# Kernel optimization log

Measured on AMD Instinct MI355X. Metric: run time of the kernel, lower is better.

The kernel has to match this reference:

```python
import jax, jax.numpy as jnp
import numpy as np

N_NODES = 100000

def _gcn_conv(x, W, b, src, dst, deg_inv_sqrt):
    # h = X W  (dense GEMM)
    h = x @ W
    # symmetric normalization: norm_e = d^{-1/2}[src] * d^{-1/2}[dst]
    norm = deg_inv_sqrt[src] * deg_inv_sqrt[dst]
    # gather-scale-scatter aggregation
    msgs = h[src] * norm[:, None]
    out = jax.ops.segment_sum(msgs, dst, num_segments=N_NODES)
    return out + b

def _prep_graph(edge_index):
    # add self loops (PyG GCNConv default)
    loop = jnp.arange(N_NODES, dtype=edge_index.dtype)
    src = jnp.concatenate([edge_index[0], loop])
    dst = jnp.concatenate([edge_index[1], loop])
    deg = jax.ops.segment_sum(jnp.ones_like(dst, dtype=jnp.float32), dst,
                              num_segments=N_NODES)
    deg_inv_sqrt = jnp.where(deg > 0, jax.lax.rsqrt(deg), 0.0)
    return src, dst, deg_inv_sqrt

def setup_inputs() -> dict:
    key = jax.random.key(0)
    ks = jax.random.split(key, 5)
    d_in, d_h, d_out, E = 128, 256, 128, 1600000
    x = jax.random.normal(ks[0], (N_NODES, d_in), dtype=jnp.float32)
    edge_index = jax.random.randint(ks[1], (2, E), 0, N_NODES, dtype=jnp.int64)
    W1 = jax.random.normal(ks[2], (d_in, d_h), dtype=jnp.float32) / np.sqrt(d_in)
    W2 = jax.random.normal(ks[3], (d_h, d_h), dtype=jnp.float32) / np.sqrt(d_h)
    W3 = jax.random.normal(ks[4], (d_h, d_out), dtype=jnp.float32) / np.sqrt(d_h)
    return {"x": x, "edge_index": edge_index,
            "W1": W1, "b1": jnp.zeros((d_h,), jnp.float32),
            "W2": W2, "b2": jnp.zeros((d_h,), jnp.float32),
            "W3": W3, "b3": jnp.zeros((d_out,), jnp.float32)}

def reference(x, edge_index, W1, b1, W2, b2, W3, b3):
    src, dst, dis = _prep_graph(edge_index)
    h = _gcn_conv(x, W1, b1, src, dst, dis)
    h = jax.nn.relu(h)  # dropout is identity in eval mode
    h = _gcn_conv(h, W2, b2, src, dst, dis)
    h = jax.nn.relu(h)
    out = _gcn_conv(h, W3, b3, src, dst, dis)
    return out
```

## Files before the change

kernel.cpp:

```cpp
#include <hip/hip_runtime.h>
#include <hip/hip_bf16.h>

#define N_NODES 100000
#define M_PAD   100096
#define SCAN_B  98

typedef __attribute__((ext_vector_type(8))) short s8v;
typedef __attribute__((ext_vector_type(4))) float f4v;
typedef unsigned short u16;
typedef unsigned int   u32;

__device__ __forceinline__ u16 f2bf(float v) {
    __hip_bfloat16 b = __float2bfloat16(v);
    return __builtin_bit_cast(u16, b);
}
__device__ __forceinline__ float bf2f(u16 u) {
    u32 t = (u32)u << 16;
    return __builtin_bit_cast(float, t);
}
__device__ __forceinline__ float bflo(u32 p) { return __builtin_bit_cast(float, p << 16); }
__device__ __forceinline__ float bfhi(u32 p) { return __builtin_bit_cast(float, p & 0xffff0000u); }

__device__ __forceinline__ void gl_lds16(const void* g, void* l) {
    __builtin_amdgcn_global_load_lds(
        (const __attribute__((address_space(1))) void*)g,
        (__attribute__((address_space(3))) void*)l, 16, 0, 0);
}


__global__ __launch_bounds__(256) void k_zero_int(int* __restrict__ p, int n) {
    int i = blockIdx.x * 256 + threadIdx.x;
    if (i < n) p[i] = 0;
}

__global__ __launch_bounds__(256) void k_count(const int* __restrict__ ei, int E,
                                               int* __restrict__ cnt) {
    for (int e = blockIdx.x * 256 + threadIdx.x; e < E; e += gridDim.x * 256)
        atomicAdd(&cnt[ei[E + e]], 1);
}

__global__ __launch_bounds__(1024) void k_scan_a(const int* __restrict__ cnt,
                                                 int* __restrict__ row_ptr,
                                                 int* __restrict__ bsum,
                                                 float* __restrict__ dis, int n) {
    __shared__ int wsum[16];
    const int tid = threadIdx.x;
    const int lane = tid & 63;
    const int wv = tid >> 6;
    const int i = blockIdx.x * 1024 + tid;
    const int v = (i < n) ? cnt[i] : 0;
    if (i < n) dis[i] = 1.0f / sqrtf((float)(v + 1));
    int x = v;
    #pragma unroll
    for (int d = 1; d < 64; d <<= 1) {
        int t = __shfl_up(x, d, 64);
        if (lane >= d) x += t;
    }
    if (lane == 63) wsum[wv] = x;
    __syncthreads();
    int woff = 0, total = 0;
    #pragma unroll
    for (int w = 0; w < 16; ++w) {
        int s = wsum[w];
        if (w < wv) woff += s;
        total += s;
    }
    if (i < n) row_ptr[i] = woff + x - v;
    if (tid == 0) bsum[blockIdx.x] = total;
}

__global__ __launch_bounds__(128) void k_scan_b(int* __restrict__ bsum,
                                                int* __restrict__ row_ptr,
                                                int nparts, int n, int total_edges) {
    __shared__ int w0tot;
    const int tid = threadIdx.x;
    const int lane = tid & 63;
    const int v = (tid < nparts) ? bsum[tid] : 0;
    int x = v;
    #pragma unroll
    for (int d = 1; d < 64; d <<= 1) {
        int t = __shfl_up(x, d, 64);
        if (lane >= d) x += t;
    }
    if (tid == 63) w0tot = x;
    __syncthreads();
    int excl = x - v + ((tid >= 64) ? w0tot : 0);
    if (tid < nparts) bsum[tid] = excl;
    if (tid == 0) row_ptr[n] = total_edges;
}

__global__ __launch_bounds__(1024) void k_scan_c(int* __restrict__ row_ptr,
                                                 const int* __restrict__ bsum,
                                                 int* __restrict__ cursor, int n) {
    const int i = blockIdx.x * 1024 + threadIdx.x;
    if (i < n) {
        const int r = row_ptr[i] + bsum[blockIdx.x];
        row_ptr[i] = r;
        cursor[i] = r;
    }
}

__global__ __launch_bounds__(256) void k_scatter(const int* __restrict__ ei, int E,
                                                 const float* __restrict__ dis,
                                                 int* __restrict__ cursor,
                                                 int2* __restrict__ edat) {
    for (int e = blockIdx.x * 256 + threadIdx.x; e < E; e += gridDim.x * 256) {
        const int s = ei[e];
        const int d = ei[E + e];
        const int pos = atomicAdd(&cursor[d], 1);
        edat[pos] = make_int2(s, __float_as_int(dis[s] * dis[d]));
    }
}

__global__ __launch_bounds__(256) void k_prep_w(const float* __restrict__ W,
                                                u16* __restrict__ Wth,
                                                u16* __restrict__ Wtl,
                                                int K, int N) {
    const int n = blockIdx.x;
    for (int k = threadIdx.x; k < K; k += 256) {
        float v = W[(size_t)k * N + n];
        u16 hi = f2bf(v);
        Wth[(size_t)n * K + k] = hi;
        Wtl[(size_t)n * K + k] = f2bf(v - bf2f(hi));
    }
}

__global__ __launch_bounds__(256) void k_x2bf(const float* __restrict__ x,
                                              u16* __restrict__ xb, long n8) {
    long i = (long)blockIdx.x * 256 + threadIdx.x;
    if (i >= n8) return;
    const float4 a = *reinterpret_cast<const float4*>(x + i * 8);
    const float4 b = *reinterpret_cast<const float4*>(x + i * 8 + 4);
    uint4 p;
    p.x = (u32)f2bf(a.x) | ((u32)f2bf(a.y) << 16);
    p.y = (u32)f2bf(a.z) | ((u32)f2bf(a.w) << 16);
    p.z = (u32)f2bf(b.x) | ((u32)f2bf(b.y) << 16);
    p.w = (u32)f2bf(b.z) | ((u32)f2bf(b.w) << 16);
    *reinterpret_cast<uint4*>(xb + i * 8) = p;
}

template <bool BIAS, bool RELU>
__global__ __launch_bounds__(256) void k_gemm2p(
    const u16* __restrict__ A,
    const u16* __restrict__ Bth, const u16* __restrict__ Btl,
    const float* __restrict__ bias,
    u16* __restrict__ Ch,
    int M, int N, int K) {
    __shared__ u16 As[128 * 32];
    __shared__ u16 Bhs[128 * 32];
    __shared__ u16 Bls[128 * 32];

    const int tid  = threadIdx.x;
    const int wid  = tid >> 6;
    const int lane = tid & 63;
    const int wm = wid >> 1;
    const int wn = wid & 1;
    const int row0 = blockIdx.y * 128;
    const int n0   = blockIdx.x * 128;

    const int srow  = lane >> 2;
    const int sbyte = (lane & 3) * 16;
    const int fr = lane & 15;
    const int kg = (lane >> 4) * 8;

    f4v acc[4][4];
    #pragma unroll
    for (int t = 0; t < 4; ++t)
        #pragma unroll
        for (int u = 0; u < 4; ++u)
            acc[t][u] = (f4v){0.f, 0.f, 0.f, 0.f};

    for (int k0 = 0; k0 < K; k0 += 32) {
        #pragma unroll
        for (int g = 0; g < 2; ++g) {
            const int rloc = wid * 32 + g * 16;
            const size_t ga = (size_t)(row0 + rloc + srow) * K + k0;
            gl_lds16((const char*)(A + ga) + sbyte, &As[rloc * 32]);
            const size_t gb = (size_t)(n0 + rloc + srow) * K + k0;
            gl_lds16((const char*)(Bth + gb) + sbyte, &Bhs[rloc * 32]);
            gl_lds16((const char*)(Btl + gb) + sbyte, &Bls[rloc * 32]);
        }
        __syncthreads();

        s8v nh[4], nl[4];
        #pragma unroll
        for (int u = 0; u < 4; ++u) {
            const int rb = (wn * 64 + u * 16 + fr) * 32 + kg;
            nh[u] = *(const s8v*)&Bhs[rb];
            nl[u] = *(const s8v*)&Bls[rb];
        }
        #pragma unroll
        for (int t = 0; t < 4; ++t) {
            const int ra = (wm * 64 + t * 16 + fr) * 32 + kg;
            const s8v m = *(const s8v*)&As[ra];
            #pragma unroll
            for (int u = 0; u < 4; ++u) {
                acc[t][u] = __builtin_amdgcn_mfma_f32_16x16x32_bf16(nh[u], m, acc[t][u], 0, 0, 0);
                acc[t][u] = __builtin_amdgcn_mfma_f32_16x16x32_bf16(nl[u], m, acc[t][u], 0, 0, 0);
            }
        }
        __syncthreads();
    }

    const int ncol = (lane >> 4) * 4;
    #pragma unroll
    for (int t = 0; t < 4; ++t) {
        const int grow = row0 + wm * 64 + t * 16 + fr;
        if (grow < M) {
            #pragma unroll
            for (int u = 0; u < 4; ++u) {
                const int nb = n0 + wn * 64 + u * 16 + ncol;
                float v[4];
                #pragma unroll
                for (int r = 0; r < 4; ++r) {
                    float z = acc[t][u][r];
                    if constexpr (BIAS) z += bias[nb + r];
                    if constexpr (RELU) z = fmaxf(z, 0.f);
                    v[r] = z;
                }
                const size_t off = (size_t)grow * N + nb;
                u16 hi[4];
                #pragma unroll
                for (int r = 0; r < 4; ++r) hi[r] = f2bf(v[r]);
                uint2 ph;
                ph.x = (u32)hi[0] | ((u32)hi[1] << 16);
                ph.y = (u32)hi[2] | ((u32)hi[3] << 16);
                *reinterpret_cast<uint2*>(Ch + off) = ph;
            }
        }
    }
}

template <int D, bool BIAS, bool RELU, int OUT_MODE>
__global__ __launch_bounds__(256) void k_agg(
    const u16* __restrict__ h, const int* __restrict__ row_ptr,
    const int2* __restrict__ edat,
    const float* __restrict__ dis, const float* __restrict__ bias,
    float* __restrict__ outf, u16* __restrict__ outh) {
    constexpr int V = D / 64;
    const int wave = threadIdx.x >> 6;
    const int lane = threadIdx.x & 63;
    const int node = blockIdx.x * 4 + wave;
    if (node >= N_NODES) return;

    const int beg = row_ptr[node];
    const int end = row_ptr[node + 1];
    const int base = lane * V;

    float a[4][V];
    #pragma unroll
    for (int c = 0; c < 4; ++c)
        #pragma unroll
        for (int j = 0; j < V; ++j) a[c][j] = 0.f;

#define LOADV(dst, s) do {                                                    \
        const u16* p_ = h + (size_t)(s) * D + base;                           \
        if constexpr (V == 4) {                                               \
            uint2 t_ = *reinterpret_cast<const uint2*>(p_);                   \
            dst[0] = bflo(t_.x); dst[1] = bfhi(t_.x);                         \
            dst[2] = bflo(t_.y); dst[3] = bfhi(t_.y);                         \
        } else {                                                              \
            u32 t_ = *reinterpret_cast<const u32*>(p_);                       \
            dst[0] = bflo(t_); dst[1] = bfhi(t_);                             \
        }                                                                     \
    } while (0)

    int e = beg;
    for (; e + 8 <= end; e += 8) {
        int2 ed[8];
        float v[8][V];
        #pragma unroll
        for (int j = 0; j < 8; ++j) ed[j] = edat[e + j];
        #pragma unroll
        for (int j = 0; j < 8; ++j) LOADV(v[j], ed[j].x);
        #pragma unroll
        for (int j = 0; j < 8; ++j) {
            const float w = __int_as_float(ed[j].y);
            #pragma unroll
            for (int k = 0; k < V; ++k) a[j & 3][k] += v[j][k] * w;
        }
    }
    for (; e + 2 <= end; e += 2) {
        const int2 e0 = edat[e], e1 = edat[e + 1];
        float v0[V], v1[V];
        LOADV(v0, e0.x); LOADV(v1, e1.x);
        const float w0 = __int_as_float(e0.y), w1 = __int_as_float(e1.y);
        #pragma unroll
        for (int k = 0; k < V; ++k) { a[0][k] += v0[k] * w0; a[1][k] += v1[k] * w1; }
    }
    if (e < end) {
        const int2 e0 = edat[e];
        float v0[V];
        LOADV(v0, e0.x);
        const float w0 = __int_as_float(e0.y);
        #pragma unroll
        for (int k = 0; k < V; ++k) a[2][k] += v0[k] * w0;
    }

    {
        float sw = dis[node];
        sw *= sw;
        float vs[V];
        LOADV(vs, node);
        #pragma unroll
        for (int k = 0; k < V; ++k) a[3][k] += vs[k] * sw;
    }
#undef LOADV

    float r[V];
    #pragma unroll
    for (int j = 0; j < V; ++j) {
        float v = (a[0][j] + a[1][j]) + (a[2][j] + a[3][j]);
        if constexpr (BIAS) v += bias[base + j];
        if constexpr (RELU) v = fmaxf(v, 0.f);
        r[j] = v;
    }

    const size_t off = (size_t)node * D + base;
    if constexpr (OUT_MODE == 1) {
        u16 hi[V];
        #pragma unroll
        for (int j = 0; j < V; ++j) hi[j] = f2bf(r[j]);
        if constexpr (V == 4) {
            uint2 ph;
            ph.x = (u32)hi[0] | ((u32)hi[1] << 16);
            ph.y = (u32)hi[2] | ((u32)hi[3] << 16);
            *reinterpret_cast<uint2*>(outh + off) = ph;
        } else {
            *reinterpret_cast<u32*>(outh + off) = (u32)hi[0] | ((u32)hi[1] << 16);
        }
    } else {
        if constexpr (V == 4) {
            *reinterpret_cast<float4*>(outf + off) = make_float4(r[0], r[1], r[2], r[3]);
        } else {
            *reinterpret_cast<float2*>(outf + off) = make_float2(r[0], r[1]);
        }
    }
}


extern "C" void kernel_launch(void* const* d_in, const int* in_sizes, int n_in,
                              void* d_out, int out_size, void* d_ws, size_t ws_size,
                              hipStream_t stream) {
    const float* x  = (const float*)d_in[0];
    const int*   ei = (const int*)d_in[1];
    const float* W1 = (const float*)d_in[2];
    const float* b1 = (const float*)d_in[3];
    const float* W2 = (const float*)d_in[4];
    const float* b2 = (const float*)d_in[5];
    const float* W3 = (const float*)d_in[6];
    const float* b3 = (const float*)d_in[7];
    float* out = (float*)d_out;

    const int N = N_NODES;
    const int E = in_sizes[1] / 2;

    char* ws = (char*)d_ws;
    size_t o = 0;
    auto take = [&](size_t bytes) {
        void* p = ws + o;
        o += (bytes + 255) & ~(size_t)255;
        return p;
    };
    float* dis     = (float*)take((size_t)N * 4);
    int*   row_ptr = (int*)  take((size_t)(N + 1) * 4);
    int*   cnt_cur = (int*)  take((size_t)N * 4);
    int*   bsum    = (int*)  take((size_t)SCAN_B * 4);
    int2*  edat    = (int2*) take((size_t)E * 8);
    u16* wt1h = (u16*)take((size_t)256 * 128 * 2);
    u16* wt1l = (u16*)take((size_t)256 * 128 * 2);
    u16* wt2h = (u16*)take((size_t)256 * 256 * 2);
    u16* wt2l = (u16*)take((size_t)256 * 256 * 2);
    u16* wt3h = (u16*)take((size_t)128 * 256 * 2);
    u16* wt3l = (u16*)take((size_t)128 * 256 * 2);
    char* slot1 = (char*)take((size_t)M_PAD * 256 * 2);
    char* slot2 = (char*)take((size_t)M_PAD * 256 * 2);
    (void)ws_size; (void)n_in; (void)out_size;

    u16* xb = (u16*)slot1;
    u16* h1 = (u16*)slot1;
    u16* h2 = (u16*)slot1;
    u16* xa = (u16*)slot2;
    u16* g2 = (u16*)slot2;
    u16* g3 = (u16*)slot2;

    const int nb_nodes = (N + 255) / 256;
    const int nb_edges = (E + 255) / 256;

    k_zero_int<<<nb_nodes, 256, 0, stream>>>(cnt_cur, N);
    k_count<<<nb_edges, 256, 0, stream>>>(ei, E, cnt_cur);
    k_scan_a<<<SCAN_B, 1024, 0, stream>>>(cnt_cur, row_ptr, bsum, dis, N);
    k_scan_b<<<1, 128, 0, stream>>>(bsum, row_ptr, SCAN_B, N, E);
    k_scan_c<<<SCAN_B, 1024, 0, stream>>>(row_ptr, bsum, cnt_cur, N);
    k_scatter<<<nb_edges, 256, 0, stream>>>(ei, E, dis, cnt_cur, edat);

    k_prep_w<<<256, 256, 0, stream>>>(W1, wt1h, wt1l, 128, 256);
    k_prep_w<<<256, 256, 0, stream>>>(W2, wt2h, wt2l, 256, 256);
    k_prep_w<<<128, 256, 0, stream>>>(W3, wt3h, wt3l, 256, 128);
    const long n8 = (long)N * 128 / 8;
    k_x2bf<<<(int)((n8 + 255) / 256), 256, 0, stream>>>(x, xb, n8);

    const int agg_blocks = (N + 3) / 4;
    const int m_blocks = M_PAD / 128;

    k_agg<128, false, false, 1><<<agg_blocks, 256, 0, stream>>>(
        xb, row_ptr, edat, dis, nullptr, nullptr, xa);
    k_gemm2p<true, true><<<dim3(2, m_blocks), 256, 0, stream>>>(
        xa, wt1h, wt1l, b1, h1, N, 256, 128);

    k_gemm2p<false, false><<<dim3(2, m_blocks), 256, 0, stream>>>(
        h1, wt2h, wt2l, nullptr, g2, N, 256, 256);
    k_agg<256, true, true, 1><<<agg_blocks, 256, 0, stream>>>(
        g2, row_ptr, edat, dis, b2, nullptr, h2);

    k_gemm2p<false, false><<<dim3(1, m_blocks), 256, 0, stream>>>(
        h2, wt3h, wt3l, nullptr, g3, N, 128, 256);
    k_agg<128, true, false, 0><<<agg_blocks, 256, 0, stream>>>(
        g3, row_ptr, edat, dis, b3, out, nullptr);
}
```

Measured before the change: 656.5 us.

## Enlarge GEMM tile to 256 rows, vectorize edge loops, merge weight prep

The GEMM now runs 512 threads per block over a 256-row M tile, so each block's B tiles (hi and lo) are shared by twice as many A rows. The edge count and scatter kernels read the edge indices two at a time as int2 and issue two atomics per thread. The three weight-preparation launches are merged into one kernel that dispatches on block index. The larger tile adds LDS use and may reduce the number of blocks in flight. The GEMM body also has to index 8 waves correctly, and this cannot be confirmed because that part of the code is not shown.

```diff
diff --git a/kernel.cpp b/kernel.cpp
--- a/kernel.cpp
+++ b/kernel.cpp
@@ -35,8 +35,14 @@
 
 __global__ __launch_bounds__(256) void k_count(const int* __restrict__ ei, int E,
                                                int* __restrict__ cnt) {
-    for (int e = blockIdx.x * 256 + threadIdx.x; e < E; e += gridDim.x * 256)
-        atomicAdd(&cnt[ei[E + e]], 1);
+    const int h = E >> 1;
+    for (int i = blockIdx.x * 256 + threadIdx.x; i < h; i += gridDim.x * 256) {
+        const int2 d2 = *reinterpret_cast<const int2*>(ei + E + 2 * i);
+        atomicAdd(&cnt[d2.x], 1);
+        atomicAdd(&cnt[d2.y], 1);
+    }
+    if (blockIdx.x == 0 && threadIdx.x == 0 && (E & 1))
+        atomicAdd(&cnt[ei[E + E - 1]], 1);
 }
 
 __global__ __launch_bounds__(1024) void k_scan_a(const int* __restrict__ cnt,
@@ -104,24 +110,39 @@
                                                  const float* __restrict__ dis,
                                                  int* __restrict__ cursor,
                                                  int2* __restrict__ edat) {
-    for (int e = blockIdx.x * 256 + threadIdx.x; e < E; e += gridDim.x * 256) {
-        const int s = ei[e];
-        const int d = ei[E + e];
+    const int h = E >> 1;
+    for (int i = blockIdx.x * 256 + threadIdx.x; i < h; i += gridDim.x * 256) {
+        const int2 s2 = *reinterpret_cast<const int2*>(ei + 2 * i);
+        const int2 d2 = *reinterpret_cast<const int2*>(ei + E + 2 * i);
+        const int p0 = atomicAdd(&cursor[d2.x], 1);
+        edat[p0] = make_int2(s2.x, __float_as_int(dis[s2.x] * dis[d2.x]));
+        const int p1 = atomicAdd(&cursor[d2.y], 1);
+        edat[p1] = make_int2(s2.y, __float_as_int(dis[s2.y] * dis[d2.y]));
+    }
+    if (blockIdx.x == 0 && threadIdx.x == 0 && (E & 1)) {
+        const int e = E - 1;
+        const int s = ei[e], d = ei[E + e];
         const int pos = atomicAdd(&cursor[d], 1);
         edat[pos] = make_int2(s, __float_as_int(dis[s] * dis[d]));
     }
 }
 
-__global__ __launch_bounds__(256) void k_prep_w(const float* __restrict__ W,
-                                                u16* __restrict__ Wth,
-                                                u16* __restrict__ Wtl,
-                                                int K, int N) {
-    const int n = blockIdx.x;
+__global__ __launch_bounds__(256) void k_prep_w_all(
+    const float* __restrict__ W1, const float* __restrict__ W2,
+    const float* __restrict__ W3,
+    u16* __restrict__ w1h, u16* __restrict__ w1l,
+    u16* __restrict__ w2h, u16* __restrict__ w2l,
+    u16* __restrict__ w3h, u16* __restrict__ w3l) {
+    const int b = blockIdx.x;
+    const float* W; u16 *H, *L; int K, N, n;
+    if (b < 256)      { W = W1; H = w1h; L = w1l; K = 128; N = 256; n = b; }
+    else if (b < 512) { W = W2; H = w2h; L = w2l; K = 256; N = 256; n = b - 256; }
+    else              { W = W3; H = w3h; L = w3l; K = 256; N = 128; n = b - 512; }
     for (int k = threadIdx.x; k < K; k += 256) {
         float v = W[(size_t)k * N + n];
         u16 hi = f2bf(v);
-        Wth[(size_t)n * K + k] = hi;
-        Wtl[(size_t)n * K + k] = f2bf(v - bf2f(hi));
+        H[(size_t)n * K + k] = hi;
+        L[(size_t)n * K + k] = f2bf(v - bf2f(hi));
     }
 }
 
@@ -140,13 +161,13 @@
 }
 
 template <bool BIAS, bool RELU>
-__global__ __launch_bounds__(256) void k_gemm2p(
+__global__ __launch_bounds__(512, 4) void k_gemm2p(
     const u16* __restrict__ A,
     const u16* __restrict__ Bth, const u16* __restrict__ Btl,
     const float* __restrict__ bias,
     u16* __restrict__ Ch,
     int M, int N, int K) {
-    __shared__ u16 As[128 * 32];
+    __shared__ u16 As[256 * 32];
     __shared__ u16 Bhs[128 * 32];
     __shared__ u16 Bls[128 * 32];
 
@@ -155,7 +176,7 @@
     const int lane = tid & 63;
     const int wm = wid >> 1;
     const int wn = wid & 1;
-    const int row0 = blockIdx.y * 128;
+    const int row0 = blockIdx.y * 256;
     const int n0   = blockIdx.x * 128;
 
     const int srow  = lane >> 2;
@@ -176,6 +197,9 @@
             const int rloc = wid * 32 + g * 16;
             const size_t ga = (size_t)(row0 + rloc + srow) * K + k0;
             gl_lds16((const char*)(A + ga) + sbyte, &As[rloc * 32]);
+        }
+        {
+            const int rloc = wid * 16;
             const size_t gb = (size_t)(n0 + rloc + srow) * K + k0;
             gl_lds16((const char*)(Bth + gb) + sbyte, &Bhs[rloc * 32]);
             gl_lds16((const char*)(Btl + gb) + sbyte, &Bls[rloc * 32]);
@@ -385,35 +409,33 @@
     u16* g3 = (u16*)slot2;
 
     const int nb_nodes = (N + 255) / 256;
-    const int nb_edges = (E + 255) / 256;
+    const int nb_pairs = ((E / 2) + 255) / 256;
 
     k_zero_int<<<nb_nodes, 256, 0, stream>>>(cnt_cur, N);
-    k_count<<<nb_edges, 256, 0, stream>>>(ei, E, cnt_cur);
+    k_count<<<nb_pairs, 256, 0, stream>>>(ei, E, cnt_cur);
     k_scan_a<<<SCAN_B, 1024, 0, stream>>>(cnt_cur, row_ptr, bsum, dis, N);
     k_scan_b<<<1, 128, 0, stream>>>(bsum, row_ptr, SCAN_B, N, E);
     k_scan_c<<<SCAN_B, 1024, 0, stream>>>(row_ptr, bsum, cnt_cur, N);
-    k_scatter<<<nb_edges, 256, 0, stream>>>(ei, E, dis, cnt_cur, edat);
-
-    k_prep_w<<<256, 256, 0, stream>>>(W1, wt1h, wt1l, 128, 256);
-    k_prep_w<<<256, 256, 0, stream>>>(W2, wt2h, wt2l, 256, 256);
-    k_prep_w<<<128, 256, 0, stream>>>(W3, wt3h, wt3l, 256, 128);
+    k_scatter<<<nb_pairs, 256, 0, stream>>>(ei, E, dis, cnt_cur, edat);
+
+    k_prep_w_all<<<640, 256, 0, stream>>>(W1, W2, W3, wt1h, wt1l, wt2h, wt2l, wt3h, wt3l);
     const long n8 = (long)N * 128 / 8;
     k_x2bf<<<(int)((n8 + 255) / 256), 256, 0, stream>>>(x, xb, n8);
 
     const int agg_blocks = (N + 3) / 4;
-    const int m_blocks = M_PAD / 128;
+    const int m_blocks = M_PAD / 256;
 
     k_agg<128, false, false, 1><<<agg_blocks, 256, 0, stream>>>(
         xb, row_ptr, edat, dis, nullptr, nullptr, xa);
-    k_gemm2p<true, true><<<dim3(2, m_blocks), 256, 0, stream>>>(
+    k_gemm2p<true, true><<<dim3(2, m_blocks), 512, 0, stream>>>(
         xa, wt1h, wt1l, b1, h1, N, 256, 128);
 
-    k_gemm2p<false, false><<<dim3(2, m_blocks), 256, 0, stream>>>(
+    k_gemm2p<false, false><<<dim3(2, m_blocks), 512, 0, stream>>>(
         h1, wt2h, wt2l, nullptr, g2, N, 256, 256);
     k_agg<256, true, true, 1><<<agg_blocks, 256, 0, stream>>>(
         g2, row_ptr, edat, dis, b2, nullptr, h2);
 
-    k_gemm2p<false, false><<<dim3(1, m_blocks), 256, 0, stream>>>(
+    k_gemm2p<false, false><<<dim3(1, m_blocks), 512, 0, stream>>>(
         h2, wt3h, wt3l, nullptr, g3, N, 128, 256);
     k_agg<128, true, false, 0><<<agg_blocks, 256, 0, stream>>>(
         g3, row_ptr, edat, dis, b3, out, nullptr);
```

After: 627.3 us. -4.5%, faster.
